# Kernel tuning notes

Hardware: AMD Instinct MI355X
Metric: run time of the kernel (lower is better)

## Reference

```python
import jax, jax.numpy as jnp
import numpy as np

D_HEAD = 64

def setup_inputs() -> dict:
    key = jax.random.key(0)
    kq, kk, kv, kc = jax.random.split(key, 4)
    B, H, T, D = 2, 16, 2048, D_HEAD
    Q = jax.random.normal(kq, (B, H, T, D), dtype=jnp.float32)
    K = jax.random.normal(kk, (B, H, T, D), dtype=jnp.float32)
    V = jax.random.normal(kv, (B, H, T, D), dtype=jnp.float32)
    # causal mask: True = attend
    mask = jnp.tril(jnp.ones((T, T), dtype=jnp.bool_))
    curvature = jax.random.normal(kc, (H, D, D), dtype=jnp.float32) * 0.02
    return {"Q": Q, "K": K, "V": V, "mask": mask, "curvature": curvature}

def reference(Q, K, V, mask, curvature):
    scale = 1.0 / np.sqrt(Q.shape[-1]).astype(np.float32)
    # per-head learned rotation of Q
    Q_rot = jnp.einsum('bhtd,hde->bhte', Q, curvature)
    scores = jnp.einsum('bhtd,bhsd->bhts', Q_rot, K) * scale  # [B,H,T,T]
    scores = jnp.where(mask[None, None, :, :], scores, -jnp.inf)
    attn = jax.nn.softmax(scores, axis=-1)
    out = jnp.einsum('bhts,bhsd->bhtd', attn, V)
    return out
```

## Files before the change

### kernel.cpp

```cpp
#include <hip/hip_runtime.h>


typedef __attribute__((ext_vector_type(8))) short short8;
typedef __attribute__((ext_vector_type(8))) unsigned short ushort8;
typedef __attribute__((ext_vector_type(4))) float f32x4;
typedef __attribute__((ext_vector_type(2))) _Float16 half2v;
typedef __attribute__((ext_vector_type(4))) _Float16 half4;
typedef __attribute__((ext_vector_type(8))) _Float16 half8;

constexpr int Tc = 2048;
constexpr int Dc = 64;
constexpr size_t REGION = (size_t)32 * Tc * Dc;

__device__ inline unsigned short f2bf(float f) {
    union { float f; unsigned u; } x; x.f = f;
    return (unsigned short)((x.u + 0x7fffu + ((x.u >> 16) & 1u)) >> 16);
}

__device__ inline half2v pkrtz(float a, float b) {
    return __builtin_bit_cast(half2v, __builtin_amdgcn_cvt_pkrtz(a, b));
}

#define MFMA_BF16_K32(a, b, c) __builtin_amdgcn_mfma_f32_16x16x32_bf16((a), (b), (c), 0, 0, 0)
#define MFMA_F16_K16(a, b, c)  __builtin_amdgcn_mfma_f32_16x16x16f16((a), (b), (c), 0, 0, 0)

typedef __attribute__((address_space(3))) unsigned int        lds_u32;
typedef const __attribute__((address_space(1))) unsigned int  glob_u32;
__device__ __attribute__((always_inline)) inline void gl_lds16(const void* g, void* l) {
    __builtin_amdgcn_global_load_lds((glob_u32*)g, (lds_u32*)l, 16, 0, 0);
}

__global__ __launch_bounds__(256, 1)
void holo_cfrag(const float* __restrict__ Cp, unsigned short* __restrict__ cfrag_g)
{
    const int t = threadIdx.x, lane = t & 63, eb = t >> 6;
    const int l15 = lane & 15, quad = lane >> 4;
    const int h = blockIdx.x;
    const float* Cg = Cp + (size_t)h * Dc * Dc;
    #pragma unroll
    for (int half = 0; half < 2; ++half) {
        short8 b;
        #pragma unroll
        for (int jj = 0; jj < 8; ++jj) {
            const int d = half * 32 + quad * 8 + jj;
            b[jj] = (short)f2bf(Cg[d * Dc + eb * 16 + l15]);
        }
        *(short8*)(&cfrag_g[(((size_t)h * 4 + eb) * 2 + half) * 512 + lane * 8]) = b;
    }
}

__global__ __launch_bounds__(256, 4)
void holo_prep8(const float* __restrict__ Qp, const float* __restrict__ Kp,
                const float* __restrict__ Vp,
                const unsigned short* __restrict__ cfrag_g,
                unsigned short* __restrict__ qfrag_g,
                unsigned short* __restrict__ kfrag_g,
                _Float16* __restrict__ vfrag_g)
{
    __shared__ unsigned short kt[64 * 72];
    __shared__ unsigned short qt[64 * 72];
    __shared__ _Float16      vt[64 * 72];
    __shared__ unsigned short pf[64 * 72];

    const int t = threadIdx.x, lane = t & 63, w = t >> 6;
    const int l15 = lane & 15, quad = lane >> 4, wb = w * 16;
    const int n = blockIdx.x, bh = n >> 5, st = n & 31, h = bh & 15;
    const int s0 = st * 64;

    const float* Qg = Qp + ((size_t)bh * Tc + s0) * Dc;
    const float* Kg = Kp + ((size_t)bh * Tc + s0) * Dc;
    const float* Vg = Vp + ((size_t)bh * Tc + s0) * Dc;

    #pragma unroll
    for (int kk = 0; kk < 4; ++kk) {
        const int flat = kk * 1024 + t * 4;
        const int r = flat >> 6, d0 = flat & 63;
        float4 kv = *(const float4*)(&Kg[flat]);
        ushort4 kp; kp.x = f2bf(kv.x); kp.y = f2bf(kv.y); kp.z = f2bf(kv.z); kp.w = f2bf(kv.w);
        *(ushort4*)(&kt[r * 72 + d0]) = kp;
        float4 qv = *(const float4*)(&Qg[flat]);
        ushort4 qp; qp.x = f2bf(qv.x); qp.y = f2bf(qv.y); qp.z = f2bf(qv.z); qp.w = f2bf(qv.w);
        *(ushort4*)(&qt[r * 72 + d0]) = qp;
        float4 vv = *(const float4*)(&Vg[flat]);
        half4 vp;
        vp[0] = (_Float16)vv.x; vp[1] = (_Float16)vv.y;
        vp[2] = (_Float16)vv.z; vp[3] = (_Float16)vv.w;
        *(half4*)(&vt[r * 72 + d0]) = vp;
    }
    __syncthreads();

    {
        const int row = wb + l15;
        ushort8 p0 = *(const ushort8*)(&kt[row * 72 + quad * 8]);
        ushort8 p1 = *(const ushort8*)(&kt[row * 72 + 32 + quad * 8]);
        unsigned short* ktile = kfrag_g + (size_t)(bh * 32 + st) * 4096;
        *(ushort8*)(&ktile[(w * 64 + lane) * 8])        = p0;
        *(ushort8*)(&ktile[2048 + (w * 64 + lane) * 8]) = p1;
    }

    {
        half8 v0, v1;
        #pragma unroll
        for (int dn = 0; dn < 2; ++dn)
            #pragma unroll
            for (int i = 0; i < 4; ++i)
                v0[dn * 4 + i] = vt[(wb + quad * 4 + i) * 72 + dn * 16 + l15];
        #pragma unroll
        for (int dn = 0; dn < 2; ++dn)
            #pragma unroll
            for (int i = 0; i < 4; ++i)
                v1[dn * 4 + i] = vt[(wb + quad * 4 + i) * 72 + (dn + 2) * 16 + l15];
        _Float16* vtile = vfrag_g + (size_t)(bh * 32 + st) * 4096;
        *(half8*)(&vtile[(w * 64 + lane) * 8])        = v0;
        *(half8*)(&vtile[2048 + (w * 64 + lane) * 8]) = v1;
    }

    {
        short8 a0 = *(const short8*)(&qt[(wb + l15) * 72 + quad * 8]);
        short8 a1 = *(const short8*)(&qt[(wb + l15) * 72 + 32 + quad * 8]);
        #pragma unroll
        for (int eb = 0; eb < 4; ++eb) {
            short8 b0 = *(const short8*)(&cfrag_g[(((size_t)h * 4 + eb) * 2 + 0) * 512 + lane * 8]);
            short8 b1 = *(const short8*)(&cfrag_g[(((size_t)h * 4 + eb) * 2 + 1) * 512 + lane * 8]);
            f32x4 c = {0.f, 0.f, 0.f, 0.f};
            c = MFMA_BF16_K32(a0, b0, c);
            c = MFMA_BF16_K32(a1, b1, c);
            #pragma unroll
            for (int i = 0; i < 4; ++i)
                pf[(wb + quad * 4 + i) * 72 + eb * 16 + l15] = f2bf(c[i] * 0.18033688f);
        }
        __threadfence_block();
        short8 fa0 = *(const short8*)(&pf[(wb + l15) * 72 + quad * 8]);
        short8 fa1 = *(const short8*)(&pf[(wb + l15) * 72 + 32 + quad * 8]);
        const size_t strip = (size_t)bh * 128 + st * 4 + w;
        *(short8*)(&qfrag_g[strip * 1024 + lane * 8]) = fa0;
        *(short8*)(&qfrag_g[strip * 1024 + 512 + lane * 8]) = fa1;
    }
}

__global__ __launch_bounds__(256, 2)
void holo_attn14(const unsigned short* __restrict__ qfrag_g,
                 const unsigned short* __restrict__ kfrag_g,
                 const _Float16* __restrict__ vfrag_g,
                 float* __restrict__ Op)
{
    __shared__ unsigned short bufK[2][4096];
    __shared__ _Float16      bufV[2][4096];

    const int t = threadIdx.x, lane = t & 63, wid = t >> 6;
    const int l15 = lane & 15, quad = lane >> 4;

    const int id = blockIdx.x;
    const int xcd = id & 7, sseq = id >> 3;
    const int qi = 31 - (sseq >> 2);
    const int bh = xcd * 4 + (sseq & 3);
    const int q0 = qi * 64;

    const char* kbase = (const char*)(kfrag_g + (size_t)bh * 32 * 4096);
    const char* vbase = (const char*)(vfrag_g + (size_t)bh * 32 * 4096);

    {
        gl_lds16(kbase + wid * 1024 + lane * 16,        &bufK[0][wid * 512]);
        gl_lds16(kbase + 4096 + wid * 1024 + lane * 16, &bufK[0][2048 + wid * 512]);
        gl_lds16(vbase + wid * 1024 + lane * 16,        &bufV[0][wid * 512]);
        gl_lds16(vbase + 4096 + wid * 1024 + lane * 16, &bufV[0][2048 + wid * 512]);
    }

    short8 qa0, qa1;
    {
        const size_t strip = (size_t)bh * 128 + qi * 4 + wid;
        qa0 = *(const short8*)(&qfrag_g[strip * 1024 + lane * 8]);
        qa1 = *(const short8*)(&qfrag_g[strip * 1024 + 512 + lane * 8]);
    }

    f32x4 o[4];
    #pragma unroll
    for (int dn = 0; dn < 4; ++dn) o[dn] = f32x4{0.f, 0.f, 0.f, 0.f};
    float l_lane = 0.f;
    const int rowg = q0 + wid * 16 + l15;

    asm volatile("s_waitcnt vmcnt(0)" ::: "memory");
    __builtin_amdgcn_sched_barrier(0);
    __syncthreads();

    int cur = 0;
    for (int j = 0; j <= qi; ++j) {
        if (j < qi) {
            const char* ks = kbase + (size_t)(j + 1) * 8192;
            const char* vs = vbase + (size_t)(j + 1) * 8192;
            const int nb = cur ^ 1;
            gl_lds16(ks + wid * 1024 + lane * 16,        &bufK[nb][wid * 512]);
            gl_lds16(ks + 4096 + wid * 1024 + lane * 16, &bufK[nb][2048 + wid * 512]);
            gl_lds16(vs + wid * 1024 + lane * 16,        &bufV[nb][wid * 512]);
            gl_lds16(vs + 4096 + wid * 1024 + lane * 16, &bufV[nb][2048 + wid * 512]);
        }

        const unsigned short* Kl = &bufK[cur][0];
        const _Float16*       Vl = &bufV[cur][0];

        f32x4 st[4];
        __builtin_amdgcn_s_setprio(1);
        #pragma unroll
        for (int tn = 0; tn < 4; ++tn) {
            short8 k0 = *(const short8*)(&Kl[(tn * 64 + lane) * 8]);
            short8 k1 = *(const short8*)(&Kl[2048 + (tn * 64 + lane) * 8]);
            f32x4 c = {0.f, 0.f, 0.f, 0.f};
            c = MFMA_BF16_K32(k0, qa0, c);
            c = MFMA_BF16_K32(k1, qa1, c);
            st[tn] = c;
        }
        __builtin_amdgcn_s_setprio(0);

        half4 pa[4];
        #pragma unroll
        for (int tn = 0; tn < 4; ++tn) {
            float p[4];
            #pragma unroll
            for (int i = 0; i < 4; ++i) {
                float sv = st[tn][i];
                if (j == qi) {
                    const int colg = j * 64 + tn * 16 + quad * 4 + i;
                    if (colg > rowg) sv = -1e30f;
                }
                p[i] = __builtin_amdgcn_exp2f(sv);
                l_lane += p[i];
            }
            half2v lo = pkrtz(p[0], p[1]), hi = pkrtz(p[2], p[3]);
            pa[tn] = __builtin_shufflevector(lo, hi, 0, 1, 2, 3);
        }

        __builtin_amdgcn_s_setprio(1);
        #pragma unroll
        for (int tn = 0; tn < 4; ++tn) {
            half8 vl = *(const half8*)(&Vl[(tn * 64 + lane) * 8]);
            half8 vh = *(const half8*)(&Vl[2048 + (tn * 64 + lane) * 8]);
            half4 vf0 = __builtin_shufflevector(vl, vl, 0, 1, 2, 3);
            half4 vf1 = __builtin_shufflevector(vl, vl, 4, 5, 6, 7);
            half4 vf2 = __builtin_shufflevector(vh, vh, 0, 1, 2, 3);
            half4 vf3 = __builtin_shufflevector(vh, vh, 4, 5, 6, 7);
            o[0] = MFMA_F16_K16(vf0, pa[tn], o[0]);
            o[1] = MFMA_F16_K16(vf1, pa[tn], o[1]);
            o[2] = MFMA_F16_K16(vf2, pa[tn], o[2]);
            o[3] = MFMA_F16_K16(vf3, pa[tn], o[3]);
        }
        __builtin_amdgcn_s_setprio(0);

        asm volatile("s_waitcnt vmcnt(0)" ::: "memory");
        __builtin_amdgcn_sched_barrier(0);
        __syncthreads();
        cur ^= 1;
    }

    l_lane += __shfl_xor(l_lane, 16);
    l_lane += __shfl_xor(l_lane, 32);
    const float inv = 1.0f / l_lane;

    float* dst = Op + ((size_t)bh * Tc + rowg) * Dc;
    #pragma unroll
    for (int dn = 0; dn < 4; ++dn) {
        float4 r;
        r.x = o[dn][0] * inv; r.y = o[dn][1] * inv;
        r.z = o[dn][2] * inv; r.w = o[dn][3] * inv;
        *(float4*)(&dst[dn * 16 + quad * 4]) = r;
    }
}

extern "C" void kernel_launch(void* const* d_in, const int* in_sizes, int n_in,
                              void* d_out, int out_size, void* d_ws, size_t ws_size,
                              hipStream_t stream) {
    const float* Q = (const float*)d_in[0];
    const float* K = (const float*)d_in[1];
    const float* V = (const float*)d_in[2];
    const float* C = (const float*)d_in[4];
    float* O = (float*)d_out;

    unsigned short* qfrag_w = (unsigned short*)d_ws;
    unsigned short* kfrag_w = qfrag_w + REGION;
    _Float16*       vfrag_w = (_Float16*)(kfrag_w + REGION);
    unsigned short* cfrag_w = (unsigned short*)(vfrag_w + REGION);

    holo_cfrag<<<dim3(16), dim3(256), 0, stream>>>(C, cfrag_w);
    holo_prep8<<<dim3(1024), dim3(256), 0, stream>>>(Q, K, V, cfrag_w, qfrag_w, kfrag_w, vfrag_w);
    holo_attn14<<<dim3(1024), dim3(256), 0, stream>>>(qfrag_w, kfrag_w, vfrag_w, O);
}
```

Baseline: 136.7 us.

## Process 128 query rows per block with two strips per wave

Each block now handles a 128-row query tile, with every wave owning two 16-row strips, so each K/V tile loaded into LDS serves twice as many queries. The grid is halved to 512 blocks, and the block-to-tile mapping pairs long and short causal rows to balance work. Waves whose diagonal comes earlier skip compute on the final tile. This roughly doubles accumulator registers per wave and halves the number of blocks, which may reduce occupancy or parallelism.

```diff
diff --git a/kernel.cpp b/kernel.cpp
--- a/kernel.cpp
+++ b/kernel.cpp
@@ -139,7 +139,7 @@
 }
 
 __global__ __launch_bounds__(256, 2)
-void holo_attn14(const unsigned short* __restrict__ qfrag_g,
+void holo_attn15(const unsigned short* __restrict__ qfrag_g,
                  const unsigned short* __restrict__ kfrag_g,
                  const _Float16* __restrict__ vfrag_g,
                  float* __restrict__ Op)
@@ -151,41 +151,46 @@
     const int l15 = lane & 15, quad = lane >> 4;
 
     const int id = blockIdx.x;
-    const int xcd = id & 7, sseq = id >> 3;
-    const int qi = 31 - (sseq >> 2);
-    const int bh = xcd * 4 + (sseq & 3);
-    const int q0 = qi * 64;
+    const int xcd = id & 7, seq = id >> 3;
+    const int u = seq & 15, v = (seq >> 4) & 1, w5 = (seq >> 5) & 1;
+    const int bh = xcd * 4 + v * 2 + w5;
+    const int p  = w5 ? u : 15 - u;
+    const int jmax  = 2 * p + 1;
+    const int jdiag = 2 * p + (wid >> 1);
 
     const char* kbase = (const char*)(kfrag_g + (size_t)bh * 32 * 4096);
     const char* vbase = (const char*)(vfrag_g + (size_t)bh * 32 * 4096);
 
-    {
-        gl_lds16(kbase + wid * 1024 + lane * 16,        &bufK[0][wid * 512]);
-        gl_lds16(kbase + 4096 + wid * 1024 + lane * 16, &bufK[0][2048 + wid * 512]);
-        gl_lds16(vbase + wid * 1024 + lane * 16,        &bufV[0][wid * 512]);
-        gl_lds16(vbase + 4096 + wid * 1024 + lane * 16, &bufV[0][2048 + wid * 512]);
-    }
-
-    short8 qa0, qa1;
-    {
-        const size_t strip = (size_t)bh * 128 + qi * 4 + wid;
-        qa0 = *(const short8*)(&qfrag_g[strip * 1024 + lane * 8]);
-        qa1 = *(const short8*)(&qfrag_g[strip * 1024 + 512 + lane * 8]);
-    }
-
-    f32x4 o[4];
-    #pragma unroll
-    for (int dn = 0; dn < 4; ++dn) o[dn] = f32x4{0.f, 0.f, 0.f, 0.f};
-    float l_lane = 0.f;
-    const int rowg = q0 + wid * 16 + l15;
+    gl_lds16(kbase + wid * 1024 + lane * 16,        &bufK[0][wid * 512]);
+    gl_lds16(kbase + 4096 + wid * 1024 + lane * 16, &bufK[0][2048 + wid * 512]);
+    gl_lds16(vbase + wid * 1024 + lane * 16,        &bufV[0][wid * 512]);
+    gl_lds16(vbase + 4096 + wid * 1024 + lane * 16, &bufV[0][2048 + wid * 512]);
+
+    short8 qa0[2], qa1[2];
+    #pragma unroll
+    for (int s2 = 0; s2 < 2; ++s2) {
+        const size_t strip = (size_t)bh * 128 + p * 8 + wid * 2 + s2;
+        qa0[s2] = *(const short8*)(&qfrag_g[strip * 1024 + lane * 8]);
+        qa1[s2] = *(const short8*)(&qfrag_g[strip * 1024 + 512 + lane * 8]);
+    }
+
+    f32x4 o[2][4];
+    #pragma unroll
+    for (int s2 = 0; s2 < 2; ++s2)
+        #pragma unroll
+        for (int dn = 0; dn < 4; ++dn) o[s2][dn] = f32x4{0.f, 0.f, 0.f, 0.f};
+    float l2[2] = {0.f, 0.f};
+
+    const int rowgA = p * 128 + wid * 32 + l15;
+    const int rowgB = rowgA + 16;
 
     asm volatile("s_waitcnt vmcnt(0)" ::: "memory");
     __builtin_amdgcn_sched_barrier(0);
     __syncthreads();
 
     int cur = 0;
-    for (int j = 0; j <= qi; ++j) {
-        if (j < qi) {
+    for (int j = 0; j <= jmax; ++j) {
+        if (j < jmax) {
             const char* ks = kbase + (size_t)(j + 1) * 8192;
             const char* vs = vbase + (size_t)(j + 1) * 8192;
             const int nb = cur ^ 1;
@@ -195,55 +200,81 @@
             gl_lds16(vs + 4096 + wid * 1024 + lane * 16, &bufV[nb][2048 + wid * 512]);
         }
 
-        const unsigned short* Kl = &bufK[cur][0];
-        const _Float16*       Vl = &bufV[cur][0];
-
-        f32x4 st[4];
-        __builtin_amdgcn_s_setprio(1);
-        #pragma unroll
-        for (int tn = 0; tn < 4; ++tn) {
-            short8 k0 = *(const short8*)(&Kl[(tn * 64 + lane) * 8]);
-            short8 k1 = *(const short8*)(&Kl[2048 + (tn * 64 + lane) * 8]);
-            f32x4 c = {0.f, 0.f, 0.f, 0.f};
-            c = MFMA_BF16_K32(k0, qa0, c);
-            c = MFMA_BF16_K32(k1, qa1, c);
-            st[tn] = c;
-        }
-        __builtin_amdgcn_s_setprio(0);
-
-        half4 pa[4];
-        #pragma unroll
-        for (int tn = 0; tn < 4; ++tn) {
-            float p[4];
-            #pragma unroll
-            for (int i = 0; i < 4; ++i) {
-                float sv = st[tn][i];
-                if (j == qi) {
-                    const int colg = j * 64 + tn * 16 + quad * 4 + i;
-                    if (colg > rowg) sv = -1e30f;
+        if (j <= jdiag) {
+            const unsigned short* Kl = &bufK[cur][0];
+            const _Float16*       Vl = &bufV[cur][0];
+
+            f32x4 stA[4], stB[4];
+            __builtin_amdgcn_s_setprio(1);
+            #pragma unroll
+            for (int tn = 0; tn < 4; ++tn) {
+                short8 k0 = *(const short8*)(&Kl[(tn * 64 + lane) * 8]);
+                short8 k1 = *(const short8*)(&Kl[2048 + (tn * 64 + lane) * 8]);
+                f32x4 cA = {0.f, 0.f, 0.f, 0.f};
+                cA = MFMA_BF16_K32(k0, qa0[0], cA);
+                cA = MFMA_BF16_K32(k1, qa1[0], cA);
+                stA[tn] = cA;
+                f32x4 cB = {0.f, 0.f, 0.f, 0.f};
+                cB = MFMA_BF16_K32(k0, qa0[1], cB);
+                cB = MFMA_BF16_K32(k1, qa1[1], cB);
+                stB[tn] = cB;
+            }
+            __builtin_amdgcn_s_setprio(0);
+
+            half4 paA[4], paB[4];
+            #pragma unroll
+            for (int tn = 0; tn < 4; ++tn) {
+                float pA[4];
+                #pragma unroll
+                for (int i = 0; i < 4; ++i) {
+                    float sv = stA[tn][i];
+                    if (j == jdiag) {
+                        const int colg = j * 64 + tn * 16 + quad * 4 + i;
+                        if (colg > rowgA) sv = -1e30f;
+                    }
+                    pA[i] = __builtin_amdgcn_exp2f(sv);
+                    l2[0] += pA[i];
                 }
-                p[i] = __builtin_amdgcn_exp2f(sv);
-                l_lane += p[i];
+                half2v lo = pkrtz(pA[0], pA[1]), hi = pkrtz(pA[2], pA[3]);
+                paA[tn] = __builtin_shufflevector(lo, hi, 0, 1, 2, 3);
             }
-            half2v lo = pkrtz(p[0], p[1]), hi = pkrtz(p[2], p[3]);
-            pa[tn] = __builtin_shufflevector(lo, hi, 0, 1, 2, 3);
-        }
-
-        __builtin_amdgcn_s_setprio(1);
-        #pragma unroll
-        for (int tn = 0; tn < 4; ++tn) {
-            half8 vl = *(const half8*)(&Vl[(tn * 64 + lane) * 8]);
-            half8 vh = *(const half8*)(&Vl[2048 + (tn * 64 + lane) * 8]);
-            half4 vf0 = __builtin_shufflevector(vl, vl, 0, 1, 2, 3);
-            half4 vf1 = __builtin_shufflevector(vl, vl, 4, 5, 6, 7);
-            half4 vf2 = __builtin_shufflevector(vh, vh, 0, 1, 2, 3);
-            half4 vf3 = __builtin_shufflevector(vh, vh, 4, 5, 6, 7);
-            o[0] = MFMA_F16_K16(vf0, pa[tn], o[0]);
-            o[1] = MFMA_F16_K16(vf1, pa[tn], o[1]);
-            o[2] = MFMA_F16_K16(vf2, pa[tn], o[2]);
-            o[3] = MFMA_F16_K16(vf3, pa[tn], o[3]);
-        }
-        __builtin_amdgcn_s_setprio(0);
+            #pragma unroll
+            for (int tn = 0; tn < 4; ++tn) {
+                float pB[4];
+                #pragma unroll
+                for (int i = 0; i < 4; ++i) {
+                    float sv = stB[tn][i];
+                    if (j == jdiag) {
+                        const int colg = j * 64 + tn * 16 + quad * 4 + i;
+                        if (colg > rowgB) sv = -1e30f;
+                    }
+                    pB[i] = __builtin_amdgcn_exp2f(sv);
+                    l2[1] += pB[i];
+                }
+                half2v lo = pkrtz(pB[0], pB[1]), hi = pkrtz(pB[2], pB[3]);
+                paB[tn] = __builtin_shufflevector(lo, hi, 0, 1, 2, 3);
+            }
+
+            __builtin_amdgcn_s_setprio(1);
+            #pragma unroll
+            for (int tn = 0; tn < 4; ++tn) {
+                half8 vl = *(const half8*)(&Vl[(tn * 64 + lane) * 8]);
+                half8 vh = *(const half8*)(&Vl[2048 + (tn * 64 + lane) * 8]);
+                half4 vf0 = __builtin_shufflevector(vl, vl, 0, 1, 2, 3);
+                half4 vf1 = __builtin_shufflevector(vl, vl, 4, 5, 6, 7);
+                half4 vf2 = __builtin_shufflevector(vh, vh, 0, 1, 2, 3);
+                half4 vf3 = __builtin_shufflevector(vh, vh, 4, 5, 6, 7);
+                o[0][0] = MFMA_F16_K16(vf0, paA[tn], o[0][0]);
+                o[0][1] = MFMA_F16_K16(vf1, paA[tn], o[0][1]);
+                o[0][2] = MFMA_F16_K16(vf2, paA[tn], o[0][2]);
+                o[0][3] = MFMA_F16_K16(vf3, paA[tn], o[0][3]);
+                o[1][0] = MFMA_F16_K16(vf0, paB[tn], o[1][0]);
+                o[1][1] = MFMA_F16_K16(vf1, paB[tn], o[1][1]);
+                o[1][2] = MFMA_F16_K16(vf2, paB[tn], o[1][2]);
+                o[1][3] = MFMA_F16_K16(vf3, paB[tn], o[1][3]);
+            }
+            __builtin_amdgcn_s_setprio(0);
+        }
 
         asm volatile("s_waitcnt vmcnt(0)" ::: "memory");
         __builtin_amdgcn_sched_barrier(0);
@@ -251,17 +282,21 @@
         cur ^= 1;
     }
 
-    l_lane += __shfl_xor(l_lane, 16);
-    l_lane += __shfl_xor(l_lane, 32);
-    const float inv = 1.0f / l_lane;
-
-    float* dst = Op + ((size_t)bh * Tc + rowg) * Dc;
-    #pragma unroll
-    for (int dn = 0; dn < 4; ++dn) {
-        float4 r;
-        r.x = o[dn][0] * inv; r.y = o[dn][1] * inv;
-        r.z = o[dn][2] * inv; r.w = o[dn][3] * inv;
-        *(float4*)(&dst[dn * 16 + quad * 4]) = r;
+    #pragma unroll
+    for (int s2 = 0; s2 < 2; ++s2) {
+        float l = l2[s2];
+        l += __shfl_xor(l, 16);
+        l += __shfl_xor(l, 32);
+        const float inv = 1.0f / l;
+        const int rowg = rowgA + s2 * 16;
+        float* dst = Op + ((size_t)bh * Tc + rowg) * Dc;
+        #pragma unroll
+        for (int dn = 0; dn < 4; ++dn) {
+            float4 r;
+            r.x = o[s2][dn][0] * inv; r.y = o[s2][dn][1] * inv;
+            r.z = o[s2][dn][2] * inv; r.w = o[s2][dn][3] * inv;
+            *(float4*)(&dst[dn * 16 + quad * 4]) = r;
+        }
     }
 }
 
@@ -281,5 +316,5 @@
 
     holo_cfrag<<<dim3(16), dim3(256), 0, stream>>>(C, cfrag_w);
     holo_prep8<<<dim3(1024), dim3(256), 0, stream>>>(Q, K, V, cfrag_w, qfrag_w, kfrag_w, vfrag_w);
-    holo_attn14<<<dim3(1024), dim3(256), 0, stream>>>(qfrag_w, kfrag_w, vfrag_w, O);
-}
+    holo_attn15<<<dim3(512), dim3(256), 0, stream>>>(qfrag_w, kfrag_w, vfrag_w, O);
+}
```

After: 157.8 us. +15.5%, slower.
